# Kernel tuning notes

Hardware: AMD Instinct MI355X
Metric: run time of the kernel (lower is better)

## Reference

```python
import jax, jax.numpy as jnp
import numpy as np

N, E = 100000, 1600000
IN, HID, NCLS = 128, 128, 64


def setup_inputs() -> dict:
    key = jax.random.key(0)
    ks = jax.random.split(key, 8)
    x = jax.random.normal(ks[0], (N, IN), jnp.float32)
    edge_index = jax.random.randint(ks[1], (2, E), 0, N, dtype=jnp.int32)
    s1 = 1.0 / np.sqrt(IN)
    s2 = 1.0 / np.sqrt(HID)
    return {
        "x": x,
        "edge_index": edge_index,
        "Wl1": jax.random.uniform(ks[2], (IN, HID), jnp.float32, -s1, s1),
        "Wr1": jax.random.uniform(ks[3], (IN, HID), jnp.float32, -s1, s1),
        "b1": jnp.zeros((HID,), jnp.float32),
        "Wl2": jax.random.uniform(ks[4], (HID, NCLS), jnp.float32, -s2, s2),
        "Wr2": jax.random.uniform(ks[5], (HID, NCLS), jnp.float32, -s2, s2),
        "b2": jnp.zeros((NCLS,), jnp.float32),
    }


def _sage_conv(x, src, dst, inv_deg, Wl, Wr, b):
    # mean-aggregate neighbor features at each destination node (PyG SAGEConv)
    agg = jax.ops.segment_sum(x[src], dst, num_segments=N)  # [N, d]
    agg = agg * inv_deg[:, None]
    # out = lin_l(mean_j x_j) + lin_r(x_i); bias lives in lin_l
    return agg @ Wl + x @ Wr + b


def reference(x, edge_index, Wl1, Wr1, b1, Wl2, Wr2, b2):
    src, dst = edge_index[0], edge_index[1]
    deg = jax.ops.segment_sum(jnp.ones((E,), jnp.float32), dst, num_segments=N)
    inv_deg = 1.0 / jnp.maximum(deg, 1.0)
    h = _sage_conv(x, src, dst, inv_deg, Wl1, Wr1, b1)
    h = jax.nn.relu(h)
    # dropout is identity at inference (training=False)
    h = _sage_conv(h, src, dst, inv_deg, Wl2, Wr2, b2)
    return jax.nn.log_softmax(h, axis=1)
```

## Files before the change

### kernel.cpp

```cpp
#include <hip/hip_runtime.h>
#include <hip/hip_bf16.h>


typedef __attribute__((ext_vector_type(8))) short short8;
typedef __attribute__((ext_vector_type(4))) float f32x4;
typedef __attribute__((ext_vector_type(2))) float f32x2;

#define NPB 512
#define BCAP 16384
#define CHUNK 8192

__device__ __forceinline__ ushort f2bf(float f) {
    unsigned u = __float_as_uint(f);
    return (ushort)((u + 0x7fff + ((u >> 16) & 1)) >> 16);
}
__device__ __forceinline__ float bflo(unsigned v) { return __uint_as_float(v << 16); }
__device__ __forceinline__ float bfhi(unsigned v) { return __uint_as_float(v & 0xffff0000u); }
__device__ __forceinline__ unsigned pk4bf(float a, float b) {
    return (unsigned)f2bf(a) | ((unsigned)f2bf(b) << 16);
}
__device__ __forceinline__ f32x2 shflx2(f32x2 v, int m) {
    f32x2 r; r[0] = __shfl_xor(v[0], m); r[1] = __shfl_xor(v[1], m); return r;
}

__device__ __forceinline__ void wfrag_one(const float* W, ushort* Wf, int i, int COLS) {
    int j = i & 7, m = (i >> 3) & 15, kc = (i >> 7) & 15, ct = i >> 11;
    Wf[i] = f2bf(W[(kc * 8 + j) * COLS + ct * 16 + m]);
}

__global__ void __launch_bounds__(256)
k1_scatter_cvtw(const int* __restrict__ src, const int* __restrict__ dst,
                int* __restrict__ bcount, unsigned* __restrict__ bbuf, int E, int NSC,
                const float* __restrict__ Wl1, const float* __restrict__ Wr1,
                const float* __restrict__ Wl2, const float* __restrict__ Wr2,
                ushort* __restrict__ Wf_l1, ushort* __restrict__ Wf_r1,
                ushort* __restrict__ Wf_l2, ushort* __restrict__ Wf_r2) {
    int tid = threadIdx.x;
    if ((int)blockIdx.x >= NSC) {
        int i = ((int)blockIdx.x - NSC) * 256 + tid;
        if (i < 16384)       wfrag_one(Wl1, Wf_l1, i, 128);
        else if (i < 32768)  wfrag_one(Wr1, Wf_r1, i - 16384, 128);
        else if (i < 40960)  wfrag_one(Wl2, Wf_l2, i - 32768, 64);
        else if (i < 49152)  wfrag_one(Wr2, Wf_r2, i - 40960, 64);
        return;
    }
    __shared__ unsigned entry[CHUNK];
    __shared__ unsigned char ebkt[CHUNK];
    __shared__ int lhist[256], lbase[256], lcur[256];
    lhist[tid] = 0;
    __syncthreads();
    int e0 = blockIdx.x * CHUNK;
    int cnt = min(CHUNK, E - e0);
    int nv = cnt >> 2;
    for (int t = tid; t < nv; t += 256) {
        int4 d4 = ((const int4*)(dst + e0))[t];
        int4 s4 = ((const int4*)(src + e0))[t];
        int i = t * 4;
        int b0 = d4.x >> 9, b1 = d4.y >> 9, b2 = d4.z >> 9, b3 = d4.w >> 9;
        entry[i + 0] = ((unsigned)s4.x << 9) | (unsigned)(d4.x & 511);
        entry[i + 1] = ((unsigned)s4.y << 9) | (unsigned)(d4.y & 511);
        entry[i + 2] = ((unsigned)s4.z << 9) | (unsigned)(d4.z & 511);
        entry[i + 3] = ((unsigned)s4.w << 9) | (unsigned)(d4.w & 511);
        ebkt[i + 0] = (unsigned char)b0; ebkt[i + 1] = (unsigned char)b1;
        ebkt[i + 2] = (unsigned char)b2; ebkt[i + 3] = (unsigned char)b3;
        atomicAdd(&lhist[b0], 1); atomicAdd(&lhist[b1], 1);
        atomicAdd(&lhist[b2], 1); atomicAdd(&lhist[b3], 1);
    }
    for (int i = (nv << 2) + tid; i < cnt; i += 256) {
        int d = dst[e0 + i], s = src[e0 + i];
        int b = d >> 9;
        entry[i] = ((unsigned)s << 9) | (unsigned)(d & 511);
        ebkt[i] = (unsigned char)b;
        atomicAdd(&lhist[b], 1);
    }
    __syncthreads();
    int h = lhist[tid];
    lbase[tid] = (h > 0) ? atomicAdd(&bcount[tid], h) : 0;
    lcur[tid] = 0;
    __syncthreads();
    for (int i = tid; i < cnt; i += 256) {
        int b = ebkt[i];
        int o = atomicAdd(&lcur[b], 1);
        bbuf[(long)b * BCAP + lbase[b] + o] = entry[i];
    }
}

template <int COLS, bool F32IN>
__device__ __forceinline__ void proj_body(int bid, int tid,
                            const void* __restrict__ xin,
                            const ushort* __restrict__ Wfl, const ushort* __restrict__ Wfr,
                            const float* __restrict__ bias,
                            unsigned char* __restrict__ p8, ushort* __restrict__ q, int N) {
    constexpr int CT = COLS / 16;
    int wave = tid >> 6, lane = tid & 63;
    int quad = lane >> 4, m = lane & 15;
    long row0 = (long)bid * 64 + wave * 16;
    long node = row0 + m;
    long arow = (node < N) ? node : (N - 1);

    f32x4 accp[CT], accq[CT];
#pragma unroll
    for (int ct = 0; ct < CT; ++ct) { accp[ct] = (f32x4)0.0f; accq[ct] = (f32x4)0.0f; }

#pragma unroll
    for (int kk = 0; kk < 128; kk += 32) {
        short8 b;
        if (F32IN) {
            const float* xf = (const float*)xin + arow * 128 + kk + quad * 8;
            float4 f0 = *(const float4*)xf;
            float4 f1 = *(const float4*)(xf + 4);
            b[0] = (short)f2bf(f0.x); b[1] = (short)f2bf(f0.y);
            b[2] = (short)f2bf(f0.z); b[3] = (short)f2bf(f0.w);
            b[4] = (short)f2bf(f1.x); b[5] = (short)f2bf(f1.y);
            b[6] = (short)f2bf(f1.z); b[7] = (short)f2bf(f1.w);
        } else {
            b = *(const short8*)((const ushort*)xin + arow * 128 + kk + quad * 8);
        }
        int kc = (kk >> 3) + quad;
#pragma unroll
        for (int ct = 0; ct < CT; ++ct) {
            long boff = (((long)(ct * 16 + kc) * 16) + m) * 8;
            short8 al = *(const short8*)(Wfl + boff);
            short8 ar = *(const short8*)(Wfr + boff);
            accp[ct] = __builtin_amdgcn_mfma_f32_16x16x32_bf16(al, b, accp[ct], 0, 0, 0);
            accq[ct] = __builtin_amdgcn_mfma_f32_16x16x32_bf16(ar, b, accq[ct], 0, 0, 0);
        }
    }

    if (node < N) {
#pragma unroll
        for (int ct = 0; ct < CT; ++ct) {
            int c0 = ct * 16 + quad * 4;
            float4 bv = *(const float4*)(bias + c0);
            float q0 = accq[ct][0] + bv.x, q1 = accq[ct][1] + bv.y;
            float q2 = accq[ct][2] + bv.z, q3 = accq[ct][3] + bv.w;
            unsigned w = (unsigned)__builtin_amdgcn_cvt_pk_fp8_f32(accp[ct][0], accp[ct][1], 0, false);
            w = (unsigned)__builtin_amdgcn_cvt_pk_fp8_f32(accp[ct][2], accp[ct][3], (int)w, true);
            *(unsigned*)(p8 + node * COLS + c0) = w;
            uint2 qw; qw.x = pk4bf(q0, q1); qw.y = pk4bf(q2, q3);
            *(uint2*)(q + node * COLS + c0) = qw;
        }
    }
}

__global__ void __launch_bounds__(256)
k2_csr_proj1(const unsigned* __restrict__ bbuf, const int* __restrict__ bcount,
             int* __restrict__ row_start, int* __restrict__ degw,
             float* __restrict__ inv_deg, int* __restrict__ ssrc, int NBcsr, int N,
             const float* __restrict__ x,
             const ushort* __restrict__ Wfl, const ushort* __restrict__ Wfr,
             const float* __restrict__ bias,
             unsigned char* __restrict__ p8, ushort* __restrict__ q) {
    int tid = threadIdx.x;
    if ((int)blockIdx.x >= NBcsr) {
        proj_body<128, true>((int)blockIdx.x - NBcsr, tid, x, Wfl, Wfr, bias, p8, q, N);
        return;
    }
    __shared__ int sdeg[NPB], lcur[NPB];
    int b = blockIdx.x;
    int node0 = b * NPB;
    sdeg[tid] = 0; sdeg[tid + 256] = 0;
    __syncthreads();
    int cnt = bcount[b];
    long base = (long)b * BCAP;
    for (int i = tid; i < cnt; i += 256)
        atomicAdd(&sdeg[bbuf[base + i] & 511], 1);
    __syncthreads();
    int c0 = sdeg[tid], c1 = sdeg[tid + 256];
    for (int off = 1; off < NPB; off <<= 1) {
        int a0 = (tid >= off) ? sdeg[tid - off] : 0;
        int a1 = (tid + 256 >= off) ? sdeg[tid + 256 - off] : 0;
        __syncthreads();
        sdeg[tid] += a0; sdeg[tid + 256] += a1;
        __syncthreads();
    }
    int rs0 = sdeg[tid] - c0;
    int rs1 = sdeg[tid + 256] - c1;
    lcur[tid] = rs0; lcur[tid + 256] = rs1;
    if (node0 + tid < N) {
        row_start[node0 + tid] = (int)(base + rs0);
        degw[node0 + tid] = c0;
        inv_deg[node0 + tid] = 1.0f / (float)(c0 > 1 ? c0 : 1);
    }
    if (node0 + tid + 256 < N) {
        row_start[node0 + tid + 256] = (int)(base + rs1);
        degw[node0 + tid + 256] = c1;
        inv_deg[node0 + tid + 256] = 1.0f / (float)(c1 > 1 ? c1 : 1);
    }
    __syncthreads();
    for (int i = tid; i < cnt; i += 256) {
        unsigned w = bbuf[base + i];
        int pos = atomicAdd(&lcur[w & 511], 1);
        ssrc[base + pos] = (int)(w >> 9);
    }
}

__global__ void __launch_bounds__(256)
agg_relu_kernel(const unsigned char* __restrict__ p8,
                const ushort* __restrict__ q,
                const int* __restrict__ ssrc,
                const int* __restrict__ row_start,
                const int* __restrict__ deg,
                const float* __restrict__ inv_deg,
                ushort* __restrict__ hb, int N) {
    int wave = threadIdx.x >> 6, lane = threadIdx.x & 63;
    int n = blockIdx.x * 4 + wave;
    if (n >= N) return;
    int g = lane >> 4, lm = lane & 15;
    int start = row_start[n], d = deg[n];
    const int* sp = ssrc + start;
    const unsigned char* pb = p8 + lm * 8;
    f32x2 a0 = (f32x2)0.f, a1 = (f32x2)0.f, a2 = (f32x2)0.f, a3 = (f32x2)0.f;
    int j = 0;
    for (; j + 16 <= d; j += 16) {
        int s0 = sp[j + g], s1 = sp[j + 4 + g], s2 = sp[j + 8 + g], s3 = sp[j + 12 + g];
        uint2 v0 = *(const uint2*)(pb + (long)s0 * 128);
        uint2 v1 = *(const uint2*)(pb + (long)s1 * 128);
        uint2 v2 = *(const uint2*)(pb + (long)s2 * 128);
        uint2 v3 = *(const uint2*)(pb + (long)s3 * 128);
#pragma unroll
        for (int t = 0; t < 4; ++t) {
            uint2 vv = (t == 0) ? v0 : (t == 1) ? v1 : (t == 2) ? v2 : v3;
            a0 += __builtin_amdgcn_cvt_pk_f32_fp8((int)vv.x, false);
            a1 += __builtin_amdgcn_cvt_pk_f32_fp8((int)vv.x, true);
            a2 += __builtin_amdgcn_cvt_pk_f32_fp8((int)vv.y, false);
            a3 += __builtin_amdgcn_cvt_pk_f32_fp8((int)vv.y, true);
        }
    }
    for (; j < d; j += 4) {
        int idx = j + g;
        int s = sp[idx < d ? idx : j];
        uint2 vv = *(const uint2*)(pb + (long)s * 128);
        if (idx < d) {
            a0 += __builtin_amdgcn_cvt_pk_f32_fp8((int)vv.x, false);
            a1 += __builtin_amdgcn_cvt_pk_f32_fp8((int)vv.x, true);
            a2 += __builtin_amdgcn_cvt_pk_f32_fp8((int)vv.y, false);
            a3 += __builtin_amdgcn_cvt_pk_f32_fp8((int)vv.y, true);
        }
    }
    a0 += shflx2(a0, 16); a1 += shflx2(a1, 16);
    a2 += shflx2(a2, 16); a3 += shflx2(a3, 16);
    a0 += shflx2(a0, 32); a1 += shflx2(a1, 32);
    a2 += shflx2(a2, 32); a3 += shflx2(a3, 32);
    if (g == 0) {
        float iv = inv_deg[n];
        uint4 qv = *(const uint4*)(q + (long)n * 128 + lm * 8);
        float h0 = fmaxf(a0[0] * iv + bflo(qv.x), 0.f);
        float h1 = fmaxf(a0[1] * iv + bfhi(qv.x), 0.f);
        float h2 = fmaxf(a1[0] * iv + bflo(qv.y), 0.f);
        float h3 = fmaxf(a1[1] * iv + bfhi(qv.y), 0.f);
        float h4 = fmaxf(a2[0] * iv + bflo(qv.z), 0.f);
        float h5 = fmaxf(a2[1] * iv + bfhi(qv.z), 0.f);
        float h6 = fmaxf(a3[0] * iv + bflo(qv.w), 0.f);
        float h7 = fmaxf(a3[1] * iv + bfhi(qv.w), 0.f);
        uint4 hw;
        hw.x = pk4bf(h0, h1); hw.y = pk4bf(h2, h3);
        hw.z = pk4bf(h4, h5); hw.w = pk4bf(h6, h7);
        *(uint4*)(hb + (long)n * 128 + lm * 8) = hw;
    }
}

__global__ void __launch_bounds__(256)
proj2_kernel(const ushort* __restrict__ hb,
             const ushort* __restrict__ Wfl, const ushort* __restrict__ Wfr,
             const float* __restrict__ bias,
             unsigned char* __restrict__ u8, ushort* __restrict__ v, int N) {
    proj_body<64, false>((int)blockIdx.x, (int)threadIdx.x, hb, Wfl, Wfr, bias, u8, v, N);
}

__global__ void __launch_bounds__(256)
agg_lsm_kernel(const unsigned char* __restrict__ u8,
               const ushort* __restrict__ v,
               const int* __restrict__ ssrc,
               const int* __restrict__ row_start,
               const int* __restrict__ deg,
               const float* __restrict__ inv_deg,
               float* __restrict__ out, int N) {
    int wave = threadIdx.x >> 6, lane = threadIdx.x & 63;
    int n = blockIdx.x * 4 + wave;
    if (n >= N) return;
    int g = lane >> 3, lm = lane & 7;
    int start = row_start[n], d = deg[n];
    const int* sp = ssrc + start;
    const unsigned char* ub = u8 + lm * 8;
    f32x2 a0 = (f32x2)0.f, a1 = (f32x2)0.f, a2 = (f32x2)0.f, a3 = (f32x2)0.f;
    int j = 0;
    for (; j + 16 <= d; j += 16) {
        int s0 = sp[j + g], s1 = sp[j + 8 + g];
        uint2 v0 = *(const uint2*)(ub + (long)s0 * 64);
        uint2 v1 = *(const uint2*)(ub + (long)s1 * 64);
#pragma unroll
        for (int t = 0; t < 2; ++t) {
            uint2 vv = (t == 0) ? v0 : v1;
            a0 += __builtin_amdgcn_cvt_pk_f32_fp8((int)vv.x, false);
            a1 += __builtin_amdgcn_cvt_pk_f32_fp8((int)vv.x, true);
            a2 += __builtin_amdgcn_cvt_pk_f32_fp8((int)vv.y, false);
            a3 += __builtin_amdgcn_cvt_pk_f32_fp8((int)vv.y, true);
        }
    }
    for (; j < d; j += 8) {
        int idx = j + g;
        int s = sp[idx < d ? idx : j];
        uint2 vv = *(const uint2*)(ub + (long)s * 64);
        if (idx < d) {
            a0 += __builtin_amdgcn_cvt_pk_f32_fp8((int)vv.x, false);
            a1 += __builtin_amdgcn_cvt_pk_f32_fp8((int)vv.x, true);
            a2 += __builtin_amdgcn_cvt_pk_f32_fp8((int)vv.y, false);
            a3 += __builtin_amdgcn_cvt_pk_f32_fp8((int)vv.y, true);
        }
    }
    a0 += shflx2(a0, 8);  a1 += shflx2(a1, 8);  a2 += shflx2(a2, 8);  a3 += shflx2(a3, 8);
    a0 += shflx2(a0, 16); a1 += shflx2(a1, 16); a2 += shflx2(a2, 16); a3 += shflx2(a3, 16);
    a0 += shflx2(a0, 32); a1 += shflx2(a1, 32); a2 += shflx2(a2, 32); a3 += shflx2(a3, 32);

    float iv = inv_deg[n];
    uint4 vv = *(const uint4*)(v + (long)n * 64 + lm * 8);
    float z0 = a0[0] * iv + bflo(vv.x), z1 = a0[1] * iv + bfhi(vv.x);
    float z2 = a1[0] * iv + bflo(vv.y), z3 = a1[1] * iv + bfhi(vv.y);
    float z4 = a2[0] * iv + bflo(vv.z), z5 = a2[1] * iv + bfhi(vv.z);
    float z6 = a3[0] * iv + bflo(vv.w), z7 = a3[1] * iv + bfhi(vv.w);
    float mx = fmaxf(fmaxf(fmaxf(z0, z1), fmaxf(z2, z3)),
                     fmaxf(fmaxf(z4, z5), fmaxf(z6, z7)));
#pragma unroll
    for (int o = 4; o > 0; o >>= 1) mx = fmaxf(mx, __shfl_xor(mx, o));
    float e = (__expf(z0 - mx) + __expf(z1 - mx)) + (__expf(z2 - mx) + __expf(z3 - mx)) +
              (__expf(z4 - mx) + __expf(z5 - mx)) + (__expf(z6 - mx) + __expf(z7 - mx));
#pragma unroll
    for (int o = 4; o > 0; o >>= 1) e += __shfl_xor(e, o);
    float ls = mx + __logf(e);
    if (g == 0) {
        float4 o0, o1;
        o0.x = z0 - ls; o0.y = z1 - ls; o0.z = z2 - ls; o0.w = z3 - ls;
        o1.x = z4 - ls; o1.y = z5 - ls; o1.z = z6 - ls; o1.w = z7 - ls;
        *(float4*)(out + (long)n * 64 + lm * 8) = o0;
        *(float4*)(out + (long)n * 64 + lm * 8 + 4) = o1;
    }
}

extern "C" void kernel_launch(void* const* d_in, const int* in_sizes, int n_in,
                              void* d_out, int out_size, void* d_ws, size_t ws_size,
                              hipStream_t stream) {
    const float* x   = (const float*)d_in[0];
    const int*   ei  = (const int*)d_in[1];
    const float* Wl1 = (const float*)d_in[2];
    const float* Wr1 = (const float*)d_in[3];
    const float* b1  = (const float*)d_in[4];
    const float* Wl2 = (const float*)d_in[5];
    const float* Wr2 = (const float*)d_in[6];
    const float* b2  = (const float*)d_in[7];

    const int N = in_sizes[0] / 128;
    const int E = in_sizes[1] / 2;
    const int* src = ei;
    const int* dst = ei + E;
    const int NB = (N + NPB - 1) / NPB;
    const int NSC = (E + CHUNK - 1) / CHUNK;

    size_t off = 0;
    auto take = [&](size_t nbytes) -> void* {
        void* ptr = (void*)((char*)d_ws + off);
        off += (nbytes + 255) & ~(size_t)255;
        return ptr;
    };
    int*      bcount    = (int*)take((size_t)NB * 4);
    unsigned* bbuf      = (unsigned*)take((size_t)NB * BCAP * 4);
    int*      row_start = (int*)take((size_t)N * 4);
    int*      degw      = (int*)take((size_t)N * 4);
    float*    inv_deg   = (float*)take((size_t)N * 4);
    int*      ssrc      = (int*)take((size_t)NB * BCAP * 4);
    unsigned char* p8   = (unsigned char*)take((size_t)N * 128);
    ushort*   q         = (ushort*)take((size_t)N * 128 * 2);
    ushort*   hb        = (ushort*)take((size_t)N * 128 * 2);
    ushort*   Wf_l1     = (ushort*)take(128 * 128 * 2);
    ushort*   Wf_r1     = (ushort*)take(128 * 128 * 2);
    ushort*   Wf_l2     = (ushort*)take(64 * 128 * 2);
    ushort*   Wf_r2     = (ushort*)take(64 * 128 * 2);
    unsigned char* u8 = p8;
    ushort*        v  = q;
    (void)ws_size; (void)n_in; (void)out_size;

    hipMemsetAsync(bcount, 0, (size_t)NB * 4, stream);

    k1_scatter_cvtw<<<NSC + 192, 256, 0, stream>>>(src, dst, bcount, bbuf, E, NSC,
                                                   Wl1, Wr1, Wl2, Wr2,
                                                   Wf_l1, Wf_r1, Wf_l2, Wf_r2);

    int P1 = (N + 63) / 64;
    k2_csr_proj1<<<NB + P1, 256, 0, stream>>>(bbuf, bcount, row_start, degw, inv_deg,
                                              ssrc, NB, N, x, Wf_l1, Wf_r1, b1, p8, q);

    agg_relu_kernel<<<(N + 3) / 4, 256, 0, stream>>>(p8, q, ssrc, row_start, degw, inv_deg, hb, N);

    proj2_kernel<<<(N + 63) / 64, 256, 0, stream>>>(hb, Wf_l2, Wf_r2, b2, u8, v, N);
    agg_lsm_kernel<<<(N + 3) / 4, 256, 0, stream>>>(u8, v, ssrc, row_start, degw, inv_deg,
                                                    (float*)d_out, N);
}
```

Measured before the change: 285.7 us.

## Move layer-1 projection into scatter kernel with LDS-staged weight fragments

Each projection block now converts the fp32 weights to bf16 MFMA fragment layout itself in shared memory, replacing the separate global weight pre-conversion pass. The layer-1 projection moves from the CSR-build kernel into the edge-scatter kernel so it runs alongside bucketing, and CSR build becomes its own kernel. Each projection block now handles 256 rows instead of 64 so the per-block weight conversion is amortised. The costs are 64KB of LDS per block in the scatter kernel, which can lower occupancy for the scatter blocks, and redundant weight conversion work in every block.

```diff
diff --git a/kernel.cpp b/kernel.cpp
--- a/kernel.cpp
+++ b/kernel.cpp
@@ -9,6 +9,7 @@
 #define NPB 512
 #define BCAP 16384
 #define CHUNK 8192
+#define RPB 256
 
 __device__ __forceinline__ ushort f2bf(float f) {
     unsigned u = __float_as_uint(f);
@@ -23,30 +24,96 @@
     f32x2 r; r[0] = __shfl_xor(v[0], m); r[1] = __shfl_xor(v[1], m); return r;
 }
 
-__device__ __forceinline__ void wfrag_one(const float* W, ushort* Wf, int i, int COLS) {
-    int j = i & 7, m = (i >> 3) & 15, kc = (i >> 7) & 15, ct = i >> 11;
-    Wf[i] = f2bf(W[(kc * 8 + j) * COLS + ct * 16 + m]);
-}
-
-__global__ void __launch_bounds__(256)
-k1_scatter_cvtw(const int* __restrict__ src, const int* __restrict__ dst,
-                int* __restrict__ bcount, unsigned* __restrict__ bbuf, int E, int NSC,
-                const float* __restrict__ Wl1, const float* __restrict__ Wr1,
-                const float* __restrict__ Wl2, const float* __restrict__ Wr2,
-                ushort* __restrict__ Wf_l1, ushort* __restrict__ Wf_r1,
-                ushort* __restrict__ Wf_l2, ushort* __restrict__ Wf_r2) {
+template <int COLS, bool F32IN>
+__device__ __forceinline__ void proj_lds(int bid, int tid, ushort* sW,
+                            const void* __restrict__ xin,
+                            const float* __restrict__ Wl, const float* __restrict__ Wr,
+                            const float* __restrict__ bias,
+                            unsigned char* __restrict__ p8, ushort* __restrict__ q, int N) {
+    constexpr int CT = COLS / 16;
+    ushort* sWl = sW;
+    ushort* sWr = sW + COLS * 128;
+    for (int t = tid; t < COLS * 128; t += 256) {
+        int k = t / COLS, c = t % COLS;
+        int dst = (((c >> 4) * 16 + (k >> 3)) * 16 + (c & 15)) * 8 + (k & 7);
+        sWl[dst] = f2bf(Wl[t]);
+        sWr[dst] = f2bf(Wr[t]);
+    }
+    __syncthreads();
+
+    int wave = tid >> 6, lane = tid & 63;
+    int quad = lane >> 4, m = lane & 15;
+#pragma unroll
+    for (int rg = 0; rg < RPB / 64; ++rg) {
+        long row0 = (long)bid * RPB + rg * 64 + wave * 16;
+        long node = row0 + m;
+        long arow = (node < N) ? node : (N - 1);
+
+        f32x4 accp[CT], accq[CT];
+#pragma unroll
+        for (int ct = 0; ct < CT; ++ct) { accp[ct] = (f32x4)0.0f; accq[ct] = (f32x4)0.0f; }
+
+#pragma unroll
+        for (int kk = 0; kk < 128; kk += 32) {
+            short8 b;
+            if (F32IN) {
+                const float* xf = (const float*)xin + arow * 128 + kk + quad * 8;
+                float4 f0 = *(const float4*)xf;
+                float4 f1 = *(const float4*)(xf + 4);
+                b[0] = (short)f2bf(f0.x); b[1] = (short)f2bf(f0.y);
+                b[2] = (short)f2bf(f0.z); b[3] = (short)f2bf(f0.w);
+                b[4] = (short)f2bf(f1.x); b[5] = (short)f2bf(f1.y);
+                b[6] = (short)f2bf(f1.z); b[7] = (short)f2bf(f1.w);
+            } else {
+                b = *(const short8*)((const ushort*)xin + arow * 128 + kk + quad * 8);
+            }
+            int kc = (kk >> 3) + quad;
+#pragma unroll
+            for (int ct = 0; ct < CT; ++ct) {
+                int boff = ((ct * 16 + kc) * 16 + m) * 8;
+                short8 al = *(const short8*)(sWl + boff);
+                short8 ar = *(const short8*)(sWr + boff);
+                accp[ct] = __builtin_amdgcn_mfma_f32_16x16x32_bf16(al, b, accp[ct], 0, 0, 0);
+                accq[ct] = __builtin_amdgcn_mfma_f32_16x16x32_bf16(ar, b, accq[ct], 0, 0, 0);
+            }
+        }
+
+        if (node < N) {
+#pragma unroll
+            for (int ct = 0; ct < CT; ++ct) {
+                int c0 = ct * 16 + quad * 4;
+                float4 bv = *(const float4*)(bias + c0);
+                float q0 = accq[ct][0] + bv.x, q1 = accq[ct][1] + bv.y;
+                float q2 = accq[ct][2] + bv.z, q3 = accq[ct][3] + bv.w;
+                unsigned w = (unsigned)__builtin_amdgcn_cvt_pk_fp8_f32(accp[ct][0], accp[ct][1], 0, false);
+                w = (unsigned)__builtin_amdgcn_cvt_pk_fp8_f32(accp[ct][2], accp[ct][3], (int)w, true);
+                *(unsigned*)(p8 + node * COLS + c0) = w;
+                uint2 qw; qw.x = pk4bf(q0, q1); qw.y = pk4bf(q2, q3);
+                *(uint2*)(q + node * COLS + c0) = qw;
+            }
+        }
+    }
+}
+
+__global__ void __launch_bounds__(256)
+k1_scatter_proj1(const int* __restrict__ src, const int* __restrict__ dst,
+                 int* __restrict__ bcount, unsigned* __restrict__ bbuf, int E, int NSC,
+                 const float* __restrict__ x,
+                 const float* __restrict__ Wl1, const float* __restrict__ Wr1,
+                 const float* __restrict__ b1,
+                 unsigned char* __restrict__ p8, ushort* __restrict__ q, int N) {
+    __shared__ __align__(16) char smem[65536];
     int tid = threadIdx.x;
     if ((int)blockIdx.x >= NSC) {
-        int i = ((int)blockIdx.x - NSC) * 256 + tid;
-        if (i < 16384)       wfrag_one(Wl1, Wf_l1, i, 128);
-        else if (i < 32768)  wfrag_one(Wr1, Wf_r1, i - 16384, 128);
-        else if (i < 40960)  wfrag_one(Wl2, Wf_l2, i - 32768, 64);
-        else if (i < 49152)  wfrag_one(Wr2, Wf_r2, i - 40960, 64);
+        proj_lds<128, true>((int)blockIdx.x - NSC, tid, (ushort*)smem,
+                            x, Wl1, Wr1, b1, p8, q, N);
         return;
     }
-    __shared__ unsigned entry[CHUNK];
-    __shared__ unsigned char ebkt[CHUNK];
-    __shared__ int lhist[256], lbase[256], lcur[256];
+    unsigned* entry = (unsigned*)smem;
+    unsigned char* ebkt = (unsigned char*)(smem + 32768);
+    int* lhist = (int*)(smem + 40960);
+    int* lbase = (int*)(smem + 41984);
+    int* lcur  = (int*)(smem + 43008);
     lhist[tid] = 0;
     __syncthreads();
     int e0 = blockIdx.x * CHUNK;
@@ -56,14 +123,14 @@
         int4 d4 = ((const int4*)(dst + e0))[t];
         int4 s4 = ((const int4*)(src + e0))[t];
         int i = t * 4;
-        int b0 = d4.x >> 9, b1 = d4.y >> 9, b2 = d4.z >> 9, b3 = d4.w >> 9;
+        int b0 = d4.x >> 9, b1_ = d4.y >> 9, b2 = d4.z >> 9, b3 = d4.w >> 9;
         entry[i + 0] = ((unsigned)s4.x << 9) | (unsigned)(d4.x & 511);
         entry[i + 1] = ((unsigned)s4.y << 9) | (unsigned)(d4.y & 511);
         entry[i + 2] = ((unsigned)s4.z << 9) | (unsigned)(d4.z & 511);
         entry[i + 3] = ((unsigned)s4.w << 9) | (unsigned)(d4.w & 511);
-        ebkt[i + 0] = (unsigned char)b0; ebkt[i + 1] = (unsigned char)b1;
+        ebkt[i + 0] = (unsigned char)b0; ebkt[i + 1] = (unsigned char)b1_;
         ebkt[i + 2] = (unsigned char)b2; ebkt[i + 3] = (unsigned char)b3;
-        atomicAdd(&lhist[b0], 1); atomicAdd(&lhist[b1], 1);
+        atomicAdd(&lhist[b0], 1); atomicAdd(&lhist[b1_], 1);
         atomicAdd(&lhist[b2], 1); atomicAdd(&lhist[b3], 1);
     }
     for (int i = (nv << 2) + tid; i < cnt; i += 256) {
@@ -85,79 +152,12 @@
     }
 }
 
-template <int COLS, bool F32IN>
-__device__ __forceinline__ void proj_body(int bid, int tid,
-                            const void* __restrict__ xin,
-                            const ushort* __restrict__ Wfl, const ushort* __restrict__ Wfr,
-                            const float* __restrict__ bias,
-                            unsigned char* __restrict__ p8, ushort* __restrict__ q, int N) {
-    constexpr int CT = COLS / 16;
-    int wave = tid >> 6, lane = tid & 63;
-    int quad = lane >> 4, m = lane & 15;
-    long row0 = (long)bid * 64 + wave * 16;
-    long node = row0 + m;
-    long arow = (node < N) ? node : (N - 1);
-
-    f32x4 accp[CT], accq[CT];
-#pragma unroll
-    for (int ct = 0; ct < CT; ++ct) { accp[ct] = (f32x4)0.0f; accq[ct] = (f32x4)0.0f; }
-
-#pragma unroll
-    for (int kk = 0; kk < 128; kk += 32) {
-        short8 b;
-        if (F32IN) {
-            const float* xf = (const float*)xin + arow * 128 + kk + quad * 8;
-            float4 f0 = *(const float4*)xf;
-            float4 f1 = *(const float4*)(xf + 4);
-            b[0] = (short)f2bf(f0.x); b[1] = (short)f2bf(f0.y);
-            b[2] = (short)f2bf(f0.z); b[3] = (short)f2bf(f0.w);
-            b[4] = (short)f2bf(f1.x); b[5] = (short)f2bf(f1.y);
-            b[6] = (short)f2bf(f1.z); b[7] = (short)f2bf(f1.w);
-        } else {
-            b = *(const short8*)((const ushort*)xin + arow * 128 + kk + quad * 8);
-        }
-        int kc = (kk >> 3) + quad;
-#pragma unroll
-        for (int ct = 0; ct < CT; ++ct) {
-            long boff = (((long)(ct * 16 + kc) * 16) + m) * 8;
-            short8 al = *(const short8*)(Wfl + boff);
-            short8 ar = *(const short8*)(Wfr + boff);
-            accp[ct] = __builtin_amdgcn_mfma_f32_16x16x32_bf16(al, b, accp[ct], 0, 0, 0);
-            accq[ct] = __builtin_amdgcn_mfma_f32_16x16x32_bf16(ar, b, accq[ct], 0, 0, 0);
-        }
-    }
-
-    if (node < N) {
-#pragma unroll
-        for (int ct = 0; ct < CT; ++ct) {
-            int c0 = ct * 16 + quad * 4;
-            float4 bv = *(const float4*)(bias + c0);
-            float q0 = accq[ct][0] + bv.x, q1 = accq[ct][1] + bv.y;
-            float q2 = accq[ct][2] + bv.z, q3 = accq[ct][3] + bv.w;
-            unsigned w = (unsigned)__builtin_amdgcn_cvt_pk_fp8_f32(accp[ct][0], accp[ct][1], 0, false);
-            w = (unsigned)__builtin_amdgcn_cvt_pk_fp8_f32(accp[ct][2], accp[ct][3], (int)w, true);
-            *(unsigned*)(p8 + node * COLS + c0) = w;
-            uint2 qw; qw.x = pk4bf(q0, q1); qw.y = pk4bf(q2, q3);
-            *(uint2*)(q + node * COLS + c0) = qw;
-        }
-    }
-}
-
-__global__ void __launch_bounds__(256)
-k2_csr_proj1(const unsigned* __restrict__ bbuf, const int* __restrict__ bcount,
-             int* __restrict__ row_start, int* __restrict__ degw,
-             float* __restrict__ inv_deg, int* __restrict__ ssrc, int NBcsr, int N,
-             const float* __restrict__ x,
-             const ushort* __restrict__ Wfl, const ushort* __restrict__ Wfr,
-             const float* __restrict__ bias,
-             unsigned char* __restrict__ p8, ushort* __restrict__ q) {
-    int tid = threadIdx.x;
-    if ((int)blockIdx.x >= NBcsr) {
-        proj_body<128, true>((int)blockIdx.x - NBcsr, tid, x, Wfl, Wfr, bias, p8, q, N);
-        return;
-    }
+__global__ void __launch_bounds__(256)
+build_csr(const unsigned* __restrict__ bbuf, const int* __restrict__ bcount,
+          int* __restrict__ row_start, int* __restrict__ degw,
+          float* __restrict__ inv_deg, int* __restrict__ ssrc, int N) {
     __shared__ int sdeg[NPB], lcur[NPB];
-    int b = blockIdx.x;
+    int b = blockIdx.x, tid = threadIdx.x;
     int node0 = b * NPB;
     sdeg[tid] = 0; sdeg[tid + 256] = 0;
     __syncthreads();
@@ -262,10 +262,11 @@
 
 __global__ void __launch_bounds__(256)
 proj2_kernel(const ushort* __restrict__ hb,
-             const ushort* __restrict__ Wfl, const ushort* __restrict__ Wfr,
-             const float* __restrict__ bias,
+             const float* __restrict__ Wl2, const float* __restrict__ Wr2,
+             const float* __restrict__ b2,
              unsigned char* __restrict__ u8, ushort* __restrict__ v, int N) {
-    proj_body<64, false>((int)blockIdx.x, (int)threadIdx.x, hb, Wfl, Wfr, bias, u8, v, N);
+    __shared__ __align__(16) ushort sW[2 * 64 * 128];
+    proj_lds<64, false>((int)blockIdx.x, (int)threadIdx.x, sW, hb, Wl2, Wr2, b2, u8, v, N);
 }
 
 __global__ void __launch_bounds__(256)
@@ -355,6 +356,7 @@
     const int* dst = ei + E;
     const int NB = (N + NPB - 1) / NPB;
     const int NSC = (E + CHUNK - 1) / CHUNK;
+    const int NP = (N + RPB - 1) / RPB;
 
     size_t off = 0;
     auto take = [&](size_t nbytes) -> void* {
@@ -371,27 +373,21 @@
     unsigned char* p8   = (unsigned char*)take((size_t)N * 128);
     ushort*   q         = (ushort*)take((size_t)N * 128 * 2);
     ushort*   hb        = (ushort*)take((size_t)N * 128 * 2);
-    ushort*   Wf_l1     = (ushort*)take(128 * 128 * 2);
-    ushort*   Wf_r1     = (ushort*)take(128 * 128 * 2);
-    ushort*   Wf_l2     = (ushort*)take(64 * 128 * 2);
-    ushort*   Wf_r2     = (ushort*)take(64 * 128 * 2);
     unsigned char* u8 = p8;
     ushort*        v  = q;
     (void)ws_size; (void)n_in; (void)out_size;
 
     hipMemsetAsync(bcount, 0, (size_t)NB * 4, stream);
 
-    k1_scatter_cvtw<<<NSC + 192, 256, 0, stream>>>(src, dst, bcount, bbuf, E, NSC,
-                                                   Wl1, Wr1, Wl2, Wr2,
-                                                   Wf_l1, Wf_r1, Wf_l2, Wf_r2);
-
-    int P1 = (N + 63) / 64;
-    k2_csr_proj1<<<NB + P1, 256, 0, stream>>>(bbuf, bcount, row_start, degw, inv_deg,
-                                              ssrc, NB, N, x, Wf_l1, Wf_r1, b1, p8, q);
+    k1_scatter_proj1<<<NSC + NP, 256, 0, stream>>>(src, dst, bcount, bbuf, E, NSC,
+                                                   x, Wl1, Wr1, b1, p8, q, N);
+
+    build_csr<<<NB, 256, 0, stream>>>(bbuf, bcount, row_start, degw, inv_deg, ssrc, N);
 
     agg_relu_kernel<<<(N + 3) / 4, 256, 0, stream>>>(p8, q, ssrc, row_start, degw, inv_deg, hb, N);
 
-    proj2_kernel<<<(N + 63) / 64, 256, 0, stream>>>(hb, Wf_l2, Wf_r2, b2, u8, v, N);
+    proj2_kernel<<<NP, 256, 0, stream>>>(hb, Wl2, Wr2, b2, u8, v, N);
+
     agg_lsm_kernel<<<(N + 3) / 4, 256, 0, stream>>>(u8, v, ssrc, row_start, degw, inv_deg,
                                                     (float*)d_out, N);
 }
```

Result: slower. 327.1 us (+14.5%).
